# Kernel tuning notes

Hardware: AMD Instinct MI355X
Metric: run time of the kernel (lower is better)

The kernel has to match this reference:

```python
import jax, jax.numpy as jnp
import numpy as np

N = 100_000
E = 1_600_000
F_IN = 128
HEADS = 8
OUT_H = 8   # per-head channels, concat -> 64
N_CLS = 40
K_HOPS = 10  # truncation order of heat-kernel Taylor series
NEG_SLOPE = 0.2
T_INIT = 5.0


def setup_inputs() -> dict:
    key = jax.random.key(0)
    ks = jax.random.split(key, 10)
    x = jax.random.normal(ks[0], (N, F_IN), jnp.float32)
    edge_index = jax.random.randint(ks[1], (2, E), 0, N, jnp.int32)
    t = jnp.full((F_IN,), T_INIT, jnp.float32)  # per-channel learnable diffusion time
    W1 = jax.random.normal(ks[2], (F_IN, HEADS * OUT_H), jnp.float32) / np.sqrt(F_IN).astype(np.float32)
    a_src1 = jax.random.normal(ks[3], (HEADS, OUT_H), jnp.float32) * 0.1
    a_dst1 = jax.random.normal(ks[4], (HEADS, OUT_H), jnp.float32) * 0.1
    b1 = jnp.zeros((HEADS * OUT_H,), jnp.float32)
    W2 = jax.random.normal(ks[5], (HEADS * OUT_H, N_CLS), jnp.float32) / np.sqrt(HEADS * OUT_H).astype(np.float32)
    a_src2 = jax.random.normal(ks[6], (1, N_CLS), jnp.float32) * 0.1
    a_dst2 = jax.random.normal(ks[7], (1, N_CLS), jnp.float32) * 0.1
    b2 = jnp.zeros((N_CLS,), jnp.float32)
    return {"x": x, "edge_index": edge_index, "t": t, "W1": W1, "a_src1": a_src1,
            "a_dst1": a_dst1, "b1": b1, "W2": W2, "a_src2": a_src2, "a_dst2": a_dst2, "b2": b2}


def _add_self_loops(edge_index, n):
    loop = jnp.arange(n, dtype=edge_index.dtype)
    return jnp.concatenate([edge_index, jnp.stack([loop, loop])], axis=1)


def _diffusion(x, src, dst, t, n):
    # heat kernel: exp(-t) * sum_k t^k/k! * A_hat^k x, per-channel t
    deg = jax.ops.segment_sum(jnp.ones_like(src, jnp.float32), dst, num_segments=n)
    dinv = jnp.where(deg > 0, jax.lax.rsqrt(jnp.maximum(deg, 1.0)), 0.0)
    norm = dinv[src] * dinv[dst]  # [E+N]

    def prop(h):
        return jax.ops.segment_sum(norm[:, None] * h[src], dst, num_segments=n)

    coef0 = jnp.exp(-t)  # [F]

    def step(carry, k):
        h, coef, acc = carry
        h = prop(h)
        coef = coef * t / k
        return (h, coef, acc + coef * h), None

    (_, _, out), _ = jax.lax.scan(step, (x, coef0, coef0 * x),
                                  jnp.arange(1, K_HOPS + 1, dtype=jnp.float32))
    return out


def _gat_layer(x, src, dst, W, a_s, a_d, b, heads, out_ch, concat, n):
    h = (x @ W).reshape(n, heads, out_ch)                  # [N,H,C]
    al_s = jnp.einsum('nhc,hc->nh', h, a_s)                # src attn logits
    al_d = jnp.einsum('nhc,hc->nh', h, a_d)
    e = jax.nn.leaky_relu(al_s[src] + al_d[dst], NEG_SLOPE)  # [E+N, H]
    emax = jax.ops.segment_max(e, dst, num_segments=n)       # stable softmax per target node
    ex = jnp.exp(e - emax[dst])
    denom = jax.ops.segment_sum(ex, dst, num_segments=n)
    alpha = ex / jnp.maximum(denom[dst], 1e-16)               # [E+N, H]
    out = jax.ops.segment_sum(alpha[:, :, None] * h[src], dst, num_segments=n)  # [N,H,C]
    out = out.reshape(n, heads * out_ch) if concat else out.mean(axis=1)
    return out + b


def reference(x, edge_index, t, W1, a_src1, a_dst1, b1, W2, a_src2, a_dst2, b2):
    n = x.shape[0]
    ei = _add_self_loops(edge_index, n)
    src, dst = ei[0], ei[1]
    h = _diffusion(x, src, dst, t, n)
    h = _gat_layer(h, src, dst, W1, a_src1, a_dst1, b1, HEADS, OUT_H, True, n)
    h = jax.nn.elu(h)
    h = _gat_layer(h, src, dst, W2, a_src2, a_dst2, b2, 1, N_CLS, False, n)
    return jax.nn.log_softmax(h, axis=1)
```

## Files before the change

### kernel.cpp

```cpp
#include <hip/hip_runtime.h>
#include <hip/hip_bf16.h>


static __device__ __forceinline__ unsigned pack_bf16x2(float a, float b) {
    __hip_bfloat162 p(__float2bfloat16(a), __float2bfloat16(b));
    return *reinterpret_cast<unsigned*>(&p);
}
static __device__ __forceinline__ float bf16lo(unsigned u) {
    return __uint_as_float(u << 16);
}
static __device__ __forceinline__ float bf16hi(unsigned u) {
    return __uint_as_float(u & 0xffff0000u);
}

__global__ void init_node_kernel(int* deg, int n) {
    int i = blockIdx.x * 256 + threadIdx.x;
    if (i < n) deg[i] = 1;
}

__global__ void edge_deg_kernel(const int* __restrict__ dst, int* deg, int* epos, int E) {
    int e = blockIdx.x * 256 + threadIdx.x;
    if (e < E) epos[e] = atomicAdd(&deg[dst[e]], 1);
}

__global__ void alloc_kernel(const int* __restrict__ deg, float* dinv,
                             int* row_off, int* gcount, int n) {
    int i = blockIdx.x * 256 + threadIdx.x;
    if (i >= n) return;
    int dg = deg[i];
    dinv[i] = rsqrtf((float)dg);
    row_off[i] = atomicAdd(gcount, dg);
}

__global__ void scatter_kernel(const int* __restrict__ ei, const int* __restrict__ row_off,
                               const int* __restrict__ epos, const float* __restrict__ dinv,
                               int2* __restrict__ csr_pair, int E, int n) {
    int e = blockIdx.x * 256 + threadIdx.x;
    if (e < E) {
        int s = ei[e], d = ei[E + e];
        csr_pair[row_off[d] + epos[e]] = make_int2(s, __float_as_int(dinv[s] * dinv[d]));
    } else if (e < E + n) {
        int i = e - E;
        float di = dinv[i];
        csr_pair[row_off[i]] = make_int2(i, __float_as_int(di * di));
    }
}

__global__ void coef_kernel(const float* __restrict__ t, float* coefs) {
    int c = threadIdx.x;
    float tc = t[c];
    float v = expf(-tc);
    coefs[c] = v;
    for (int k = 1; k <= 10; ++k) { v *= tc / (float)k; coefs[k * 128 + c] = v; }
}

__global__ void init_diff_kernel(const float4* __restrict__ x4, uint2* __restrict__ h0,
                                 int total4) {
    int i = blockIdx.x * 256 + threadIdx.x;
    if (i >= total4) return;
    float4 xv = x4[i];
    h0[i] = make_uint2(pack_bf16x2(xv.x, xv.y), pack_bf16x2(xv.z, xv.w));
}

static __device__ __forceinline__ float2 gather_row(
    const int* __restrict__ row_off, const int* __restrict__ deg,
    const int2* __restrict__ csr_pair, const unsigned* __restrict__ h,
    int wid, int lane) {
    int off = row_off[wid];
    int cnt = deg[wid];
    float2 a0 = {0.f, 0.f}, a1 = {0.f, 0.f}, a2 = {0.f, 0.f}, a3 = {0.f, 0.f};
    for (int base = 0; base < cnt; base += 64) {
        int nb = min(64, cnt - base);
        int2 p = {0, 0};
        if (lane < nb) p = csr_pair[off + base + lane];
        int tt = 0;
        for (; tt + 7 < nb; tt += 8) {
            int s0 = __builtin_amdgcn_readlane(p.x, tt);
            int s1 = __builtin_amdgcn_readlane(p.x, tt + 1);
            int s2 = __builtin_amdgcn_readlane(p.x, tt + 2);
            int s3 = __builtin_amdgcn_readlane(p.x, tt + 3);
            int s4 = __builtin_amdgcn_readlane(p.x, tt + 4);
            int s5 = __builtin_amdgcn_readlane(p.x, tt + 5);
            int s6 = __builtin_amdgcn_readlane(p.x, tt + 6);
            int s7 = __builtin_amdgcn_readlane(p.x, tt + 7);
            float w0 = __int_as_float(__builtin_amdgcn_readlane(p.y, tt));
            float w1 = __int_as_float(__builtin_amdgcn_readlane(p.y, tt + 1));
            float w2 = __int_as_float(__builtin_amdgcn_readlane(p.y, tt + 2));
            float w3 = __int_as_float(__builtin_amdgcn_readlane(p.y, tt + 3));
            float w4 = __int_as_float(__builtin_amdgcn_readlane(p.y, tt + 4));
            float w5 = __int_as_float(__builtin_amdgcn_readlane(p.y, tt + 5));
            float w6 = __int_as_float(__builtin_amdgcn_readlane(p.y, tt + 6));
            float w7 = __int_as_float(__builtin_amdgcn_readlane(p.y, tt + 7));
            unsigned u0 = h[(size_t)s0 * 64 + lane];
            unsigned u1 = h[(size_t)s1 * 64 + lane];
            unsigned u2 = h[(size_t)s2 * 64 + lane];
            unsigned u3 = h[(size_t)s3 * 64 + lane];
            unsigned u4 = h[(size_t)s4 * 64 + lane];
            unsigned u5 = h[(size_t)s5 * 64 + lane];
            unsigned u6 = h[(size_t)s6 * 64 + lane];
            unsigned u7 = h[(size_t)s7 * 64 + lane];
            a0.x = fmaf(w0, bf16lo(u0), a0.x); a0.y = fmaf(w0, bf16hi(u0), a0.y);
            a1.x = fmaf(w1, bf16lo(u1), a1.x); a1.y = fmaf(w1, bf16hi(u1), a1.y);
            a2.x = fmaf(w2, bf16lo(u2), a2.x); a2.y = fmaf(w2, bf16hi(u2), a2.y);
            a3.x = fmaf(w3, bf16lo(u3), a3.x); a3.y = fmaf(w3, bf16hi(u3), a3.y);
            a0.x = fmaf(w4, bf16lo(u4), a0.x); a0.y = fmaf(w4, bf16hi(u4), a0.y);
            a1.x = fmaf(w5, bf16lo(u5), a1.x); a1.y = fmaf(w5, bf16hi(u5), a1.y);
            a2.x = fmaf(w6, bf16lo(u6), a2.x); a2.y = fmaf(w6, bf16hi(u6), a2.y);
            a3.x = fmaf(w7, bf16lo(u7), a3.x); a3.y = fmaf(w7, bf16hi(u7), a3.y);
        }
        for (; tt < nb; ++tt) {
            int s = __builtin_amdgcn_readlane(p.x, tt);
            float w = __int_as_float(__builtin_amdgcn_readlane(p.y, tt));
            unsigned u = h[(size_t)s * 64 + lane];
            a0.x = fmaf(w, bf16lo(u), a0.x); a0.y = fmaf(w, bf16hi(u), a0.y);
        }
    }
    float2 s;
    s.x = (a0.x + a1.x) + (a2.x + a3.x);
    s.y = (a0.y + a1.y) + (a2.y + a3.y);
    return s;
}

__global__ void hop_kernel(const int* __restrict__ row_off, const int* __restrict__ deg,
                           const int2* __restrict__ csr_pair,
                           const unsigned* __restrict__ h_prev, unsigned* __restrict__ h_out,
                           int n) {
    int wid = (blockIdx.x << 2) + (threadIdx.x >> 6);
    int lane = threadIdx.x & 63;
    if (wid >= n) return;
    float2 s = gather_row(row_off, deg, csr_pair, h_prev, wid, lane);
    h_out[(size_t)wid * 64 + lane] = pack_bf16x2(s.x, s.y);
}

__global__ void acc_first_kernel(const float4* __restrict__ x4,
                                 const uint2* __restrict__ hA, const uint2* __restrict__ hB,
                                 const float* __restrict__ coefs,
                                 float4* __restrict__ acc4, int total4) {
    int i = blockIdx.x * 256 + threadIdx.x;
    if (i >= total4) return;
    int c4 = (i & 31) * 4;
    const float4 c0 = *(const float4*)&coefs[c4];
    const float4 cA = *(const float4*)&coefs[128 + c4];
    const float4 cB = *(const float4*)&coefs[256 + c4];
    float4 xv = x4[i];
    uint2 ua = hA[i];
    uint2 ub = hB[i];
    float4 a;
    a.x = c0.x * xv.x + cA.x * bf16lo(ua.x) + cB.x * bf16lo(ub.x);
    a.y = c0.y * xv.y + cA.y * bf16hi(ua.x) + cB.y * bf16hi(ub.x);
    a.z = c0.z * xv.z + cA.z * bf16lo(ua.y) + cB.z * bf16lo(ub.y);
    a.w = c0.w * xv.w + cA.w * bf16hi(ua.y) + cB.w * bf16hi(ub.y);
    acc4[i] = a;
}

__global__ void acc_pair_kernel(const uint2* __restrict__ hA, const uint2* __restrict__ hB,
                                const float* __restrict__ coefA, const float* __restrict__ coefB,
                                float4* __restrict__ acc4, int total4) {
    int i = blockIdx.x * 256 + threadIdx.x;
    if (i >= total4) return;
    int c4 = (i & 31) * 4;
    const float4 cA = *(const float4*)&coefA[c4];
    const float4 cB = *(const float4*)&coefB[c4];
    uint2 ua = hA[i];
    uint2 ub = hB[i];
    float4 a = acc4[i];
    a.x += cA.x * bf16lo(ua.x) + cB.x * bf16lo(ub.x);
    a.y += cA.y * bf16hi(ua.x) + cB.y * bf16hi(ub.x);
    a.z += cA.z * bf16lo(ua.y) + cB.z * bf16lo(ub.y);
    a.w += cA.w * bf16hi(ua.y) + cB.w * bf16hi(ub.y);
    acc4[i] = a;
}

__global__ __launch_bounds__(256) void gemm1_kernel(
    const float* __restrict__ acc, const float* __restrict__ W1,
    const float* __restrict__ a_s, const float* __restrict__ a_d,
    unsigned* __restrict__ h1b, float* __restrict__ als, float* __restrict__ ald, int n) {
    __shared__ unsigned short Wl16[128 * 64];
    __shared__ unsigned Al[4][16 * 64];
    for (int i = threadIdx.x; i < 128 * 64; i += 256)
        Wl16[i] = (unsigned short)(pack_bf16x2(W1[i], 0.f) & 0xffffu);
    int w = threadIdx.x >> 6;
    int lane = threadIdx.x & 63;
    int node0 = (blockIdx.x * 4 + w) * 16;
    const float2* acc2 = (const float2*)acc;
#pragma unroll
    for (int i = 0; i < 16; ++i) {
        int node = node0 + i;
        float2 v = (node < n) ? acc2[(size_t)node * 64 + lane] : make_float2(0.f, 0.f);
        Al[w][i * 64 + lane] = pack_bf16x2(v.x, v.y);
    }
    __syncthreads();
    float sums[16];
#pragma unroll
    for (int nd = 0; nd < 16; ++nd) sums[nd] = 0.f;
#pragma unroll 1
    for (int kc = 0; kc < 16; ++kc) {
        float wr[8];
#pragma unroll
        for (int i = 0; i < 8; ++i)
            wr[i] = __uint_as_float((unsigned)Wl16[(kc * 8 + i) * 64 + lane] << 16);
#pragma unroll
        for (int nd = 0; nd < 16; ++nd) {
            uint4 u = *(const uint4*)&Al[w][nd * 64 + kc * 4];
            float s = sums[nd];
            s = fmaf(wr[0], bf16lo(u.x), s); s = fmaf(wr[1], bf16hi(u.x), s);
            s = fmaf(wr[2], bf16lo(u.y), s); s = fmaf(wr[3], bf16hi(u.y), s);
            s = fmaf(wr[4], bf16lo(u.z), s); s = fmaf(wr[5], bf16hi(u.z), s);
            s = fmaf(wr[6], bf16lo(u.w), s); s = fmaf(wr[7], bf16hi(u.w), s);
            sums[nd] = s;
        }
    }
    float asv = a_s[lane], adv = a_d[lane];
#pragma unroll
    for (int nd = 0; nd < 16; ++nd) {
        int node = node0 + nd;
        if (node >= n) break;
        float sum = sums[nd];
        float partner = __shfl_xor(sum, 1);
        if ((lane & 1) == 0) h1b[(size_t)node * 32 + (lane >> 1)] = pack_bf16x2(sum, partner);
        float vs = sum * asv;
        float vd = sum * adv;
        vs += __shfl_xor(vs, 1); vs += __shfl_xor(vs, 2); vs += __shfl_xor(vs, 4);
        vd += __shfl_xor(vd, 1); vd += __shfl_xor(vd, 2); vd += __shfl_xor(vd, 4);
        if ((lane & 7) == 0) {
            als[(size_t)node * 8 + (lane >> 3)] = vs;
            ald[(size_t)node * 8 + (lane >> 3)] = vd;
        }
    }
}

__global__ void agg1_kernel(const int* __restrict__ row_off, const int* __restrict__ deg,
                            const int2* __restrict__ csr_pair,
                            const unsigned* __restrict__ h1b, const float* __restrict__ als,
                            const float* __restrict__ ald, const float* __restrict__ b1,
                            float2* __restrict__ helu2, int n) {
    int wid = (blockIdx.x << 2) + (threadIdx.x >> 6);
    int lane = threadIdx.x & 63;
    if (wid >= n) return;
    int half = lane >> 5;
    int l = lane & 31;
    int head = l >> 2;
    int off = row_off[wid];
    int cnt = deg[wid];
    float aldv = ald[(size_t)wid * 8 + head];
    float dA = 0.f, dB = 0.f;
    float2 aA = {0.f, 0.f}, aB = {0.f, 0.f};
    for (int base = 0; base < cnt; base += 64) {
        int nb = min(64, cnt - base);
        int srcv = 0;
        if (lane < nb) srcv = csr_pair[off + base + lane].x;
        int j = 0;
        for (; j + 3 < nb; j += 4) {
            int sA0 = __builtin_amdgcn_readlane(srcv, j);
            int sA1 = __builtin_amdgcn_readlane(srcv, j + 1);
            int sB0 = __builtin_amdgcn_readlane(srcv, j + 2);
            int sB1 = __builtin_amdgcn_readlane(srcv, j + 3);
            int sA = half ? sA1 : sA0;
            int sB = half ? sB1 : sB0;
            float eA = als[(size_t)sA * 8 + head] + aldv;
            float eB = als[(size_t)sB * 8 + head] + aldv;
            eA = eA > 0.f ? eA : 0.2f * eA;
            eB = eB > 0.f ? eB : 0.2f * eB;
            float pA = __expf(eA);
            float pB = __expf(eB);
            unsigned uA = h1b[(size_t)sA * 32 + l];
            unsigned uB = h1b[(size_t)sB * 32 + l];
            dA += pA; dB += pB;
            aA.x = fmaf(pA, bf16lo(uA), aA.x);
            aA.y = fmaf(pA, bf16hi(uA), aA.y);
            aB.x = fmaf(pB, bf16lo(uB), aB.x);
            aB.y = fmaf(pB, bf16hi(uB), aB.y);
        }
        for (; j < nb; j += 2) {
            int s0 = __builtin_amdgcn_readlane(srcv, j);
            int s1 = (j + 1 < nb) ? __builtin_amdgcn_readlane(srcv, j + 1) : -1;
            int s = half ? s1 : s0;
            bool valid = s >= 0;
            int ss = valid ? s : 0;
            float e = als[(size_t)ss * 8 + head] + aldv;
            e = e > 0.f ? e : 0.2f * e;
            float p = valid ? __expf(e) : 0.f;
            unsigned u = h1b[(size_t)ss * 32 + l];
            dA += p;
            aA.x = fmaf(p, bf16lo(u), aA.x);
            aA.y = fmaf(p, bf16hi(u), aA.y);
        }
    }
    float d = dA + dB;
    float2 accv = make_float2(aA.x + aB.x, aA.y + aB.y);
    d += __shfl_xor(d, 32);
    accv.x += __shfl_xor(accv.x, 32);
    accv.y += __shfl_xor(accv.y, 32);
    if (half == 0) {
        float inv = 1.f / d;
        float ox = fmaf(accv.x, inv, b1[2 * l]);
        float oy = fmaf(accv.y, inv, b1[2 * l + 1]);
        ox = ox > 0.f ? ox : expm1f(ox);
        oy = oy > 0.f ? oy : expm1f(oy);
        helu2[(size_t)wid * 32 + l] = make_float2(ox, oy);
    }
}

__global__ __launch_bounds__(256) void gemm2_kernel(
    const float* __restrict__ helu, const float* __restrict__ W2,
    const float* __restrict__ a_s, const float* __restrict__ a_d,
    unsigned* __restrict__ h2b, float* __restrict__ als, float* __restrict__ ald, int n) {
    __shared__ float Wl[64 * 40];
    __shared__ float Al[4][16 * 64];
    for (int i = threadIdx.x; i < 64 * 40; i += 256) Wl[i] = W2[i];
    int w = threadIdx.x >> 6;
    int lane = threadIdx.x & 63;
    int node0 = (blockIdx.x * 4 + w) * 16;
    const float4* hv4 = (const float4*)helu;
    float4* Av4 = (float4*)Al[w];
#pragma unroll
    for (int i = 0; i < 4; ++i) {
        int f4 = i * 64 + lane;
        int g4 = node0 * 16 + f4;
        float4 v = (g4 < n * 16) ? hv4[g4] : make_float4(0.f, 0.f, 0.f, 0.f);
        Av4[f4] = v;
    }
    __syncthreads();
    bool act = lane < 40;
    int li = act ? lane : 0;
    float sums[16];
#pragma unroll
    for (int nd = 0; nd < 16; ++nd) sums[nd] = 0.f;
#pragma unroll 1
    for (int kc = 0; kc < 8; ++kc) {
        float wr[8];
#pragma unroll
        for (int i = 0; i < 8; ++i) wr[i] = Wl[(kc * 8 + i) * 40 + li];
#pragma unroll
        for (int nd = 0; nd < 16; ++nd) {
            float4 a = *(const float4*)&Al[w][nd * 64 + kc * 8];
            float4 b = *(const float4*)&Al[w][nd * 64 + kc * 8 + 4];
            float s = sums[nd];
            s = fmaf(wr[0], a.x, s); s = fmaf(wr[1], a.y, s);
            s = fmaf(wr[2], a.z, s); s = fmaf(wr[3], a.w, s);
            s = fmaf(wr[4], b.x, s); s = fmaf(wr[5], b.y, s);
            s = fmaf(wr[6], b.z, s); s = fmaf(wr[7], b.w, s);
            sums[nd] = s;
        }
    }
    float asv = act ? a_s[lane] : 0.f;
    float adv = act ? a_d[lane] : 0.f;
#pragma unroll
    for (int nd = 0; nd < 16; ++nd) {
        int node = node0 + nd;
        if (node >= n) break;
        float sum = sums[nd];
        float partner = __shfl_xor(sum, 1);
        if (act && (lane & 1) == 0) h2b[(size_t)node * 20 + (lane >> 1)] = pack_bf16x2(sum, partner);
        float vs = act ? sum * asv : 0.f;
        float vd = act ? sum * adv : 0.f;
#pragma unroll
        for (int i = 32; i >= 1; i >>= 1) { vs += __shfl_xor(vs, i); vd += __shfl_xor(vd, i); }
        if (lane == 0) { als[node] = vs; ald[node] = vd; }
    }
}

__global__ void agg2_kernel(const int* __restrict__ row_off, const int* __restrict__ deg,
                            const int2* __restrict__ csr_pair,
                            const unsigned* __restrict__ h2b, const float* __restrict__ als,
                            const float* __restrict__ ald, const float* __restrict__ b2,
                            float* __restrict__ out, int n) {
    int wid = (blockIdx.x << 2) + (threadIdx.x >> 6);
    int lane = threadIdx.x & 63;
    if (wid >= n) return;
    int half = lane >> 5;
    int l = lane & 31;
    bool act = l < 20;
    int li = act ? l : 0;
    int off = row_off[wid];
    int cnt = deg[wid];
    float aldv = ald[wid];
    float dA = 0.f, dB = 0.f;
    float2 aA = {0.f, 0.f}, aB = {0.f, 0.f};
    for (int base = 0; base < cnt; base += 64) {
        int nb = min(64, cnt - base);
        int srcv = 0;
        if (lane < nb) srcv = csr_pair[off + base + lane].x;
        int j = 0;
        for (; j + 3 < nb; j += 4) {
            int sA0 = __builtin_amdgcn_readlane(srcv, j);
            int sA1 = __builtin_amdgcn_readlane(srcv, j + 1);
            int sB0 = __builtin_amdgcn_readlane(srcv, j + 2);
            int sB1 = __builtin_amdgcn_readlane(srcv, j + 3);
            int sA = half ? sA1 : sA0;
            int sB = half ? sB1 : sB0;
            float eA = als[sA] + aldv;
            float eB = als[sB] + aldv;
            eA = eA > 0.f ? eA : 0.2f * eA;
            eB = eB > 0.f ? eB : 0.2f * eB;
            float pA = __expf(eA);
            float pB = __expf(eB);
            unsigned uA = h2b[(size_t)sA * 20 + li];
            unsigned uB = h2b[(size_t)sB * 20 + li];
            dA += pA; dB += pB;
            aA.x = fmaf(pA, bf16lo(uA), aA.x);
            aA.y = fmaf(pA, bf16hi(uA), aA.y);
            aB.x = fmaf(pB, bf16lo(uB), aB.x);
            aB.y = fmaf(pB, bf16hi(uB), aB.y);
        }
        for (; j < nb; j += 2) {
            int s0 = __builtin_amdgcn_readlane(srcv, j);
            int s1 = (j + 1 < nb) ? __builtin_amdgcn_readlane(srcv, j + 1) : -1;
            int s = half ? s1 : s0;
            bool valid = s >= 0;
            int ss = valid ? s : 0;
            float e = als[ss] + aldv;
            e = e > 0.f ? e : 0.2f * e;
            float p = valid ? __expf(e) : 0.f;
            unsigned u = h2b[(size_t)ss * 20 + li];
            dA += p;
            aA.x = fmaf(p, bf16lo(u), aA.x);
            aA.y = fmaf(p, bf16hi(u), aA.y);
        }
    }
    float d = dA + dB;
    float2 accv = make_float2(aA.x + aB.x, aA.y + aB.y);
    d += __shfl_xor(d, 32);
    accv.x += __shfl_xor(accv.x, 32);
    accv.y += __shfl_xor(accv.y, 32);
    float inv = 1.f / d;
    bool live = (half == 0) && act;
    float ox = live ? fmaf(accv.x, inv, b2[2 * l]) : -1e30f;
    float oy = live ? fmaf(accv.y, inv, b2[2 * l + 1]) : -1e30f;
    float vv = fmaxf(ox, oy);
#pragma unroll
    for (int i = 16; i >= 1; i >>= 1) vv = fmaxf(vv, __shfl_xor(vv, i));
    float ex = live ? (__expf(ox - vv) + __expf(oy - vv)) : 0.f;
#pragma unroll
    for (int i = 16; i >= 1; i >>= 1) ex += __shfl_xor(ex, i);
    if (live) {
        float lse = vv + logf(ex);
        *(float2*)&out[(size_t)wid * 40 + 2 * l] = make_float2(ox - lse, oy - lse);
    }
}

extern "C" void kernel_launch(void* const* d_in, const int* in_sizes, int n_in,
                              void* d_out, int out_size, void* d_ws, size_t ws_size,
                              hipStream_t stream) {
    const float* x    = (const float*)d_in[0];
    const int*   ei   = (const int*)d_in[1];
    const float* t    = (const float*)d_in[2];
    const float* W1   = (const float*)d_in[3];
    const float* a_s1 = (const float*)d_in[4];
    const float* a_d1 = (const float*)d_in[5];
    const float* b1   = (const float*)d_in[6];
    const float* W2   = (const float*)d_in[7];
    const float* a_s2 = (const float*)d_in[8];
    const float* a_d2 = (const float*)d_in[9];
    const float* b2   = (const float*)d_in[10];
    float* out = (float*)d_out;

    const int N = in_sizes[0] / 128;
    const int E = in_sizes[1] / 2;

    char* w = (char*)d_ws;
    auto carve = [&](size_t bytes) {
        void* p = (void*)w;
        w += (bytes + 255) & ~(size_t)255;
        return p;
    };
    int*      deg      = (int*)carve((size_t)N * 4);
    int*      row_off  = (int*)carve((size_t)N * 4);
    int*      gcount   = (int*)carve(256);
    float*    dinv     = (float*)carve((size_t)N * 4);
    int*      epos     = (int*)carve((size_t)E * 4);
    int2*     csr_pair = (int2*)carve((size_t)(E + N) * 8);
    float*    coefs    = (float*)carve(11 * 128 * 4);
    float*    als1     = (float*)carve((size_t)N * 8 * 4);
    float*    ald1     = (float*)carve((size_t)N * 8 * 4);
    float*    als2     = (float*)carve((size_t)N * 4);
    float*    ald2     = (float*)carve((size_t)N * 4);
    float*    acc      = (float*)carve((size_t)N * 128 * 4);
    unsigned* hA       = (unsigned*)carve((size_t)N * 64 * 4);
    unsigned* hB       = (unsigned*)carve((size_t)N * 64 * 4);
    unsigned* h1b      = (unsigned*)carve((size_t)N * 32 * 4);
    float*    helu     = (float*)carve((size_t)N * 64 * 4);
    unsigned* h2b      = (unsigned*)carve((size_t)N * 20 * 4);

    dim3 blk(256);
    int gN = (N + 255) / 256;
    int gE = (E + 255) / 256;
    int gEN = (E + N + 255) / 256;
    int gW = (N + 3) / 4;
    int gT = (N + 63) / 64;
    int gS = (N * 32 + 255) / 256;

    init_node_kernel<<<gN, blk, 0, stream>>>(deg, N);
    hipMemsetAsync(gcount, 0, 4, stream);
    edge_deg_kernel<<<gE, blk, 0, stream>>>(ei + E, deg, epos, E);
    alloc_kernel<<<gN, blk, 0, stream>>>(deg, dinv, row_off, gcount, N);
    scatter_kernel<<<gEN, blk, 0, stream>>>(ei, row_off, epos, dinv, csr_pair, E, N);
    coef_kernel<<<1, 128, 0, stream>>>(t, coefs);
    init_diff_kernel<<<gS, blk, 0, stream>>>((const float4*)x, (uint2*)hA, N * 32);

    unsigned* hc = hA;
    unsigned* hn = hB;
    for (int k = 1; k <= 10; ++k) {
        hop_kernel<<<gW, blk, 0, stream>>>(row_off, deg, csr_pair, hc, hn, N);
        unsigned* tmp = hc; hc = hn; hn = tmp;
        if (k == 2) {
            acc_first_kernel<<<gS, blk, 0, stream>>>(
                (const float4*)x, (const uint2*)hB, (const uint2*)hA, coefs,
                (float4*)acc, N * 32);
        } else if ((k & 1) == 0) {
            acc_pair_kernel<<<gS, blk, 0, stream>>>(
                (const uint2*)hB, (const uint2*)hA,
                coefs + (size_t)(k - 1) * 128, coefs + (size_t)k * 128,
                (float4*)acc, N * 32);
        }
    }

    gemm1_kernel<<<gT, blk, 0, stream>>>(acc, W1, a_s1, a_d1, h1b, als1, ald1, N);
    agg1_kernel<<<gW, blk, 0, stream>>>(row_off, deg, csr_pair, h1b, als1, ald1, b1,
                                        (float2*)helu, N);
    gemm2_kernel<<<gT, blk, 0, stream>>>(helu, W2, a_s2, a_d2, h2b, als2, ald2, N);
    agg2_kernel<<<gW, blk, 0, stream>>>(row_off, deg, csr_pair, h2b, als2, ald2, b2, out, N);
}
```

Baseline: 1.259 ms.

## Fuse Taylor accumulation into even hop kernels and precompute agg2 attention per lane

```diff
diff --git a/kernel.cpp b/kernel.cpp
--- a/kernel.cpp
+++ b/kernel.cpp
@@ -11,6 +11,9 @@
 }
 static __device__ __forceinline__ float bf16hi(unsigned u) {
     return __uint_as_float(u & 0xffff0000u);
+}
+static __device__ __forceinline__ float readlane_f(float v, int l) {
+    return __int_as_float(__builtin_amdgcn_readlane(__float_as_int(v), l));
 }
 
 __global__ void init_node_kernel(int* deg, int n) {
@@ -132,43 +135,35 @@
     h_out[(size_t)wid * 64 + lane] = pack_bf16x2(s.x, s.y);
 }
 
-__global__ void acc_first_kernel(const float4* __restrict__ x4,
-                                 const uint2* __restrict__ hA, const uint2* __restrict__ hB,
-                                 const float* __restrict__ coefs,
-                                 float4* __restrict__ acc4, int total4) {
-    int i = blockIdx.x * 256 + threadIdx.x;
-    if (i >= total4) return;
-    int c4 = (i & 31) * 4;
-    const float4 c0 = *(const float4*)&coefs[c4];
-    const float4 cA = *(const float4*)&coefs[128 + c4];
-    const float4 cB = *(const float4*)&coefs[256 + c4];
-    float4 xv = x4[i];
-    uint2 ua = hA[i];
-    uint2 ub = hB[i];
-    float4 a;
-    a.x = c0.x * xv.x + cA.x * bf16lo(ua.x) + cB.x * bf16lo(ub.x);
-    a.y = c0.y * xv.y + cA.y * bf16hi(ua.x) + cB.y * bf16hi(ub.x);
-    a.z = c0.z * xv.z + cA.z * bf16lo(ua.y) + cB.z * bf16lo(ub.y);
-    a.w = c0.w * xv.w + cA.w * bf16hi(ua.y) + cB.w * bf16hi(ub.y);
-    acc4[i] = a;
-}
-
-__global__ void acc_pair_kernel(const uint2* __restrict__ hA, const uint2* __restrict__ hB,
-                                const float* __restrict__ coefA, const float* __restrict__ coefB,
-                                float4* __restrict__ acc4, int total4) {
-    int i = blockIdx.x * 256 + threadIdx.x;
-    if (i >= total4) return;
-    int c4 = (i & 31) * 4;
-    const float4 cA = *(const float4*)&coefA[c4];
-    const float4 cB = *(const float4*)&coefB[c4];
-    uint2 ua = hA[i];
-    uint2 ub = hB[i];
-    float4 a = acc4[i];
-    a.x += cA.x * bf16lo(ua.x) + cB.x * bf16lo(ub.x);
-    a.y += cA.y * bf16hi(ua.x) + cB.y * bf16hi(ub.x);
-    a.z += cA.z * bf16lo(ua.y) + cB.z * bf16lo(ub.y);
-    a.w += cA.w * bf16hi(ua.y) + cB.w * bf16hi(ub.y);
-    acc4[i] = a;
+__global__ void hop_acc_kernel(const int* __restrict__ row_off, const int* __restrict__ deg,
+                               const int2* __restrict__ csr_pair,
+                               const unsigned* __restrict__ h_prev, unsigned* __restrict__ h_out,
+                               const float2* __restrict__ x2, float2* __restrict__ acc2,
+                               const float2* __restrict__ coefPrev2,
+                               const float2* __restrict__ coefCur2,
+                               const float2* __restrict__ coef02,
+                               int n, int first, int write_h) {
+    int wid = (blockIdx.x << 2) + (threadIdx.x >> 6);
+    int lane = threadIdx.x & 63;
+    if (wid >= n) return;
+    float2 s = gather_row(row_off, deg, csr_pair, h_prev, wid, lane);
+    size_t o = (size_t)wid * 64 + lane;
+    if (write_h) h_out[o] = pack_bf16x2(s.x, s.y);
+    unsigned up = h_prev[o];
+    float2 cP = coefPrev2[lane];
+    float2 cC = coefCur2[lane];
+    float2 a;
+    if (first) {
+        float2 xv = x2[o];
+        float2 c0 = coef02[lane];
+        a.x = c0.x * xv.x;
+        a.y = c0.y * xv.y;
+    } else {
+        a = acc2[o];
+    }
+    a.x += cP.x * bf16lo(up) + cC.x * s.x;
+    a.y += cP.y * bf16hi(up) + cC.y * s.y;
+    acc2[o] = a;
 }
 
 __global__ __launch_bounds__(256) void gemm1_kernel(
@@ -380,21 +375,26 @@
     for (int base = 0; base < cnt; base += 64) {
         int nb = min(64, cnt - base);
         int srcv = 0;
-        if (lane < nb) srcv = csr_pair[off + base + lane].x;
-        int j = 0;
-        for (; j + 3 < nb; j += 4) {
+        float pv = 0.f;
+        if (lane < nb) {
+            srcv = csr_pair[off + base + lane].x;
+            float e = als[srcv] + aldv;
+            e = e > 0.f ? e : 0.2f * e;
+            pv = __expf(e);
+        }
+        for (int j = 0; j < nb; j += 4) {
             int sA0 = __builtin_amdgcn_readlane(srcv, j);
             int sA1 = __builtin_amdgcn_readlane(srcv, j + 1);
             int sB0 = __builtin_amdgcn_readlane(srcv, j + 2);
             int sB1 = __builtin_amdgcn_readlane(srcv, j + 3);
+            float pA0 = readlane_f(pv, j);
+            float pA1 = readlane_f(pv, j + 1);
+            float pB0 = readlane_f(pv, j + 2);
+            float pB1 = readlane_f(pv, j + 3);
             int sA = half ? sA1 : sA0;
             int sB = half ? sB1 : sB0;
-            float eA = als[sA] + aldv;
-            float eB = als[sB] + aldv;
-            eA = eA > 0.f ? eA : 0.2f * eA;
-            eB = eB > 0.f ? eB : 0.2f * eB;
-            float pA = __expf(eA);
-            float pB = __expf(eB);
+            float pA = half ? pA1 : pA0;
+            float pB = half ? pB1 : pB0;
             unsigned uA = h2b[(size_t)sA * 20 + li];
             unsigned uB = h2b[(size_t)sB * 20 + li];
             dA += pA; dB += pB;
@@ -402,20 +402,6 @@
             aA.y = fmaf(pA, bf16hi(uA), aA.y);
             aB.x = fmaf(pB, bf16lo(uB), aB.x);
             aB.y = fmaf(pB, bf16hi(uB), aB.y);
-        }
-        for (; j < nb; j += 2) {
-            int s0 = __builtin_amdgcn_readlane(srcv, j);
-            int s1 = (j + 1 < nb) ? __builtin_amdgcn_readlane(srcv, j + 1) : -1;
-            int s = half ? s1 : s0;
-            bool valid = s >= 0;
-            int ss = valid ? s : 0;
-            float e = als[ss] + aldv;
-            e = e > 0.f ? e : 0.2f * e;
-            float p = valid ? __expf(e) : 0.f;
-            unsigned u = h2b[(size_t)ss * 20 + li];
-            dA += p;
-            aA.x = fmaf(p, bf16lo(u), aA.x);
-            aA.y = fmaf(p, bf16hi(u), aA.y);
         }
     }
     float d = dA + dB;
@@ -501,18 +487,16 @@
     unsigned* hc = hA;
     unsigned* hn = hB;
     for (int k = 1; k <= 10; ++k) {
-        hop_kernel<<<gW, blk, 0, stream>>>(row_off, deg, csr_pair, hc, hn, N);
+        if (k & 1) {
+            hop_kernel<<<gW, blk, 0, stream>>>(row_off, deg, csr_pair, hc, hn, N);
+        } else {
+            hop_acc_kernel<<<gW, blk, 0, stream>>>(
+                row_off, deg, csr_pair, hc, hn, (const float2*)x, (float2*)acc,
+                (const float2*)(coefs + (size_t)(k - 1) * 128),
+                (const float2*)(coefs + (size_t)k * 128),
+                (const float2*)coefs, N, k == 2 ? 1 : 0, k < 10 ? 1 : 0);
+        }
         unsigned* tmp = hc; hc = hn; hn = tmp;
-        if (k == 2) {
-            acc_first_kernel<<<gS, blk, 0, stream>>>(
-                (const float4*)x, (const uint2*)hB, (const uint2*)hA, coefs,
-                (float4*)acc, N * 32);
-        } else if ((k & 1) == 0) {
-            acc_pair_kernel<<<gS, blk, 0, stream>>>(
-                (const uint2*)hB, (const uint2*)hA,
-                coefs + (size_t)(k - 1) * 128, coefs + (size_t)k * 128,
-                (float4*)acc, N * 32);
-        }
     }
 
     gemm1_kernel<<<gT, blk, 0, stream>>>(acc, W1, a_s1, a_d1, h1b, als1, ald1, N);
```

Result: faster. 1.217 ms (-3.4%).
